# Kernel optimization log

Measured on AMD Instinct MI355X. Metric: run time of the kernel, lower is better.

## Reference

```python
import jax, jax.numpy as jnp
import numpy as np

D_MODEL = 1024
N_HEADS = 16
D_HEAD = D_MODEL // N_HEADS


def setup_inputs() -> dict:
    key = jax.random.key(0)
    ks = jax.random.split(key, 5)
    s_in = 1.0 / np.sqrt(D_MODEL)
    x = jax.random.normal(ks[0], (4, 2048, D_MODEL), dtype=jnp.float32)
    W_qkv = jax.random.uniform(ks[1], (D_MODEL, 3 * D_MODEL), jnp.float32, -s_in, s_in)
    b_qkv = jax.random.uniform(ks[2], (3 * D_MODEL,), jnp.float32, -s_in, s_in)
    W_out = jax.random.uniform(ks[3], (D_MODEL, D_MODEL), jnp.float32, -s_in, s_in)
    b_out = jax.random.uniform(ks[4], (D_MODEL,), jnp.float32, -s_in, s_in)
    return {"x": x, "W_qkv": W_qkv, "b_qkv": b_qkv, "W_out": W_out, "b_out": b_out}


def reference(x, W_qkv, b_qkv, W_out, b_out):
    B, T, C = x.shape
    qkv = x @ W_qkv + b_qkv                       # [B,T,3C]
    q, k, v = jnp.split(qkv, 3, axis=-1)
    # [B,T,C] -> [B,H,T,Dh]
    def heads(t):
        return t.reshape(B, T, N_HEADS, D_HEAD).transpose(0, 2, 1, 3)
    q, k, v = heads(q), heads(k), heads(v)
    scale = 1.0 / np.sqrt(D_HEAD).astype(np.float32)
    attn = jnp.einsum('bhqd,bhkd->bhqk', q, k) * scale   # [B,H,T,T]
    causal = jnp.tril(jnp.ones((T, T), dtype=bool))
    attn = jnp.where(causal, attn, -jnp.inf)
    attn_weights = jax.nn.softmax(attn, axis=-1)
    out = jnp.einsum('bhqk,bhkd->bhqd', attn_weights, v)  # [B,H,T,Dh]
    out = out.transpose(0, 2, 1, 3).reshape(B, T, C)
    return out @ W_out + b_out
```

## Files before the change

kernel.cpp:

```cpp
#include <hip/hip_runtime.h>
#include <hip/hip_bf16.h>

#define BATCH   4
#define SEQ     2048
#define DMODEL  1024
#define NHEADS  16
#define DHEAD   64
#define MROWS   (BATCH*SEQ)
#define QKV_N   (3*DMODEL)
#define NEG_BIG (-1.0e30f)
#define WS_NEED ((size_t)MROWS * 2*DMODEL * sizeof(__hip_bfloat16))
#define SCALE_Q 0.18033688011112042f

using bf16 = __hip_bfloat16;
typedef __attribute__((ext_vector_type(8))) short short8;
typedef __attribute__((ext_vector_type(4))) float floatx4;

__device__ __align__(16) unsigned short g_wqT[QKV_N * DMODEL];
__device__ __align__(16) unsigned short g_woT[DMODEL * DMODEL];
__device__ __align__(16) unsigned short g_xb [MROWS * DMODEL];

__device__ __forceinline__ unsigned short f2bf_rne(float f) {
    union { bf16 b; unsigned short u; } t;
    t.b = __float2bfloat16(f);
    return t.u;
}

__device__ __forceinline__ void gload_lds16(const void* g, void* l) {
    __builtin_amdgcn_global_load_lds(
        (const __attribute__((address_space(1))) unsigned*)g,
        (__attribute__((address_space(3))) unsigned*)l, 16, 0, 0);
}

__global__ __launch_bounds__(256) void cast_x(const float* __restrict__ x) {
    const size_t i = ((size_t)blockIdx.x*256 + threadIdx.x)*8;
    const float4 a = *(const float4*)(x + i);
    const float4 b = *(const float4*)(x + i + 4);
    union { uint4 u4; unsigned short us[8]; } o;
    o.us[0]=f2bf_rne(a.x); o.us[1]=f2bf_rne(a.y); o.us[2]=f2bf_rne(a.z); o.us[3]=f2bf_rne(a.w);
    o.us[4]=f2bf_rne(b.x); o.us[5]=f2bf_rne(b.y); o.us[6]=f2bf_rne(b.z); o.us[7]=f2bf_rne(b.w);
    *(uint4*)(g_xb + i) = o.u4;
}

__global__ __launch_bounds__(256) void transcast_w(
    const float* __restrict__ W, int N, int which)
{
    unsigned short* dst = which ? g_woT : g_wqT;
    __shared__ unsigned short T[64][72];
    const int n0 = blockIdx.x * 64, k0 = blockIdx.y * 64;
    const int tid = threadIdx.x;
    const int r = tid >> 2, c0 = (tid & 3) * 16;

#pragma unroll
    for (int it = 0; it < 4; ++it) {
        const float4 v = *(const float4*)(W + (size_t)(k0 + r)*N + n0 + c0 + it*4);
        T[r][c0 + it*4 + 0] = f2bf_rne(v.x);
        T[r][c0 + it*4 + 1] = f2bf_rne(v.y);
        T[r][c0 + it*4 + 2] = f2bf_rne(v.z);
        T[r][c0 + it*4 + 3] = f2bf_rne(v.w);
    }
    __syncthreads();
    const int nr = tid >> 2, kc0 = (tid & 3) * 16;
#pragma unroll
    for (int it = 0; it < 2; ++it) {
        union { uint4 u4; unsigned short us[8]; } o;
#pragma unroll
        for (int j = 0; j < 8; j++) o.us[j] = T[kc0 + it*8 + j][nr];
        *(uint4*)(dst + (size_t)(n0 + nr)*DMODEL + k0 + kc0 + it*8) = o.u4;
    }
}

template<int QKV_MODE>
__global__ __launch_bounds__(512, 2) void gemm256x128(
    const void* __restrict__ Av, const float* __restrict__ bias,
    void* __restrict__ C0, void* __restrict__ C1, void* __restrict__ C2)
{
    const unsigned short* A  = QKV_MODE ? g_xb  : (const unsigned short*)Av;
    const unsigned short* BT = QKV_MODE ? g_wqT : g_woT;
    constexpr int NBN = QKV_MODE ? 24 : 8;
    constexpr int NWG = NBN * 32;

    __shared__ __align__(16) char smem[98304];
    char* const sA = smem;
    char* const sB = smem + 65536;

    const int orig = blockIdx.x;
    const int wgid = (orig & 7) * (NWG >> 3) + (orig >> 3);
    const int bm = wgid / NBN, bn = wgid % NBN;

    const int tid  = threadIdx.x;
    const int w    = tid >> 6, lane = tid & 63;
    const int m16  = lane & 15, quad = lane >> 4;
    const int rw   = w >> 1, cw = w & 1;

    const int rL = lane >> 2;
    const int cD = (lane & 3) ^ ((lane >> 3) & 3);
    const unsigned short* gA = A  + (size_t)(bm*256 + rL)*DMODEL + cD*8;
    const unsigned short* gB = BT + (size_t)(bn*128 + rL)*DMODEL + cD*8;

    const int laneRd = m16*64 + (quad ^ ((m16 >> 1) & 3))*16;

    floatx4 acc[2][2][4];
#pragma unroll
    for (int q = 0; q < 2; ++q)
#pragma unroll
        for (int i = 0; i < 2; ++i)
#pragma unroll
            for (int j = 0; j < 4; ++j) {
                acc[q][i][j][0]=0.f; acc[q][i][j][1]=0.f;
                acc[q][i][j][2]=0.f; acc[q][i][j][3]=0.f;
            }

    auto stageA = [&](int buf, int a, int k0) {
        const int rg = 4*a + (w >> 1), kh = w & 1;
        gload_lds16(gA + (size_t)(rg*16)*DMODEL + k0 + kh*32,
                    sA + buf*32768 + (rg*2 + kh)*1024);
    };
    auto stageB = [&](int buf, int b, int k0) {
        const int rg = 4*b + (w >> 1), kh = w & 1;
        gload_lds16(gB + (size_t)(rg*16)*DMODEL + k0 + kh*32,
                    sB + buf*16384 + (rg*2 + kh)*1024);
    };

    stageB(0, 0, 0); stageB(0, 1, 0);
    stageA(0, 0, 0); stageA(0, 1, 0); stageA(0, 2, 0); stageA(0, 3, 0);
    asm volatile("s_waitcnt vmcnt(0)" ::: "memory");
    __builtin_amdgcn_s_barrier();

    const int NT = DMODEL / 64;
    for (int t = 0; t < NT; ++t) {
        const int  buf = t & 1;
        const int  k1  = (t + 1) * 64;
        const bool st  = (t + 1 < NT);
        char* const Ab = sA + buf*32768;
        char* const Bb = sB + buf*16384;

        short8 bf[4][2], af[2][2];
#pragma unroll
        for (int j = 0; j < 4; ++j)
#pragma unroll
            for (int kh = 0; kh < 2; ++kh)
                bf[j][kh] = *(const short8*)(Bb + ((cw*4 + j)*2 + kh)*1024 + laneRd);
#pragma unroll
        for (int i = 0; i < 2; ++i)
#pragma unroll
            for (int kh = 0; kh < 2; ++kh)
                af[i][kh] = *(const short8*)(Ab + ((rw*2 + i)*2 + kh)*1024 + laneRd);

        if (st) { stageB(buf^1, 0, k1); stageB(buf^1, 1, k1); }
        __builtin_amdgcn_s_barrier();

        __builtin_amdgcn_s_setprio(1);
#pragma unroll
        for (int i = 0; i < 2; ++i)
#pragma unroll
            for (int j = 0; j < 4; ++j) {
                acc[0][i][j] = __builtin_amdgcn_mfma_f32_16x16x32_bf16(
                    af[i][0], bf[j][0], acc[0][i][j], 0, 0, 0);
                acc[0][i][j] = __builtin_amdgcn_mfma_f32_16x16x32_bf16(
                    af[i][1], bf[j][1], acc[0][i][j], 0, 0, 0);
            }
        __builtin_amdgcn_s_setprio(0);

        if (st) { asm volatile("s_waitcnt vmcnt(2)" ::: "memory"); }
        else    { asm volatile("s_waitcnt vmcnt(0)" ::: "memory"); }
        __builtin_amdgcn_s_barrier();

#pragma unroll
        for (int i = 0; i < 2; ++i)
#pragma unroll
            for (int kh = 0; kh < 2; ++kh)
                af[i][kh] = *(const short8*)(Ab + ((8 + rw*2 + i)*2 + kh)*1024 + laneRd);

        if (st) { stageA(buf^1, 0, k1); stageA(buf^1, 1, k1);
                  stageA(buf^1, 2, k1); stageA(buf^1, 3, k1); }
        __builtin_amdgcn_s_barrier();

        __builtin_amdgcn_s_setprio(1);
#pragma unroll
        for (int i = 0; i < 2; ++i)
#pragma unroll
            for (int j = 0; j < 4; ++j) {
                acc[1][i][j] = __builtin_amdgcn_mfma_f32_16x16x32_bf16(
                    af[i][0], bf[j][0], acc[1][i][j], 0, 0, 0);
                acc[1][i][j] = __builtin_amdgcn_mfma_f32_16x16x32_bf16(
                    af[i][1], bf[j][1], acc[1][i][j], 0, 0, 0);
            }
        __builtin_amdgcn_s_setprio(0);

        if (st) { asm volatile("s_waitcnt vmcnt(2)" ::: "memory"); }
        else    { asm volatile("s_waitcnt vmcnt(0)" ::: "memory"); }
        __builtin_amdgcn_s_barrier();
    }

    float bv[4];
#pragma unroll
    for (int j = 0; j < 4; ++j)
        bv[j] = bias[bn*128 + cw*64 + j*16 + m16];

    if (QKV_MODE) {
        const int seg = bn >> 3;
        if (seg < 2) {
            bf16* Cout = (bf16*)(seg ? C1 : C0);
            const float sc = seg ? 1.0f : SCALE_Q;
#pragma unroll
            for (int q = 0; q < 2; ++q)
#pragma unroll
                for (int i = 0; i < 2; ++i)
#pragma unroll
                    for (int r = 0; r < 4; ++r) {
                        const int gm = bm*256 + q*128 + rw*32 + i*16 + quad*4 + r;
#pragma unroll
                        for (int j = 0; j < 4; ++j) {
                            const int cc = ((bn & 7)*128 + cw*64 + j*16 + m16);
                            Cout[(size_t)gm*DMODEL + cc] =
                                __float2bfloat16((acc[q][i][j][r] + bv[j]) * sc);
                        }
                    }
        } else {
            bf16* VT = (bf16*)C2;
#pragma unroll
            for (int q = 0; q < 2; ++q)
#pragma unroll
                for (int i = 0; i < 2; ++i) {
                    const int gm0 = bm*256 + q*128 + rw*32 + i*16 + quad*4;
                    const int bb = gm0 >> 11, t0 = gm0 & 2047;
#pragma unroll
                    for (int j = 0; j < 4; ++j) {
                        const int cv = (bn & 7)*128 + cw*64 + j*16 + m16;
                        const int hh = cv >> 6, dd = cv & 63;
                        union { unsigned long long u8; unsigned short us[4]; } o;
#pragma unroll
                        for (int r = 0; r < 4; ++r)
                            o.us[r] = f2bf_rne(acc[q][i][j][r] + bv[j]);
                        *(unsigned long long*)(VT
                            + ((size_t)((bb*NHEADS + hh)*DHEAD + dd))*SEQ + t0) = o.u8;
                    }
                }
        }
    } else {
        float* Cout = (float*)C0;
#pragma unroll
        for (int q = 0; q < 2; ++q)
#pragma unroll
            for (int i = 0; i < 2; ++i)
#pragma unroll
                for (int r = 0; r < 4; ++r) {
                    const int gm = bm*256 + q*128 + rw*32 + i*16 + quad*4 + r;
#pragma unroll
                    for (int j = 0; j < 4; ++j) {
                        const int cc = bn*128 + cw*64 + j*16 + m16;
                        Cout[(size_t)gm*DMODEL + cc] = acc[q][i][j][r] + bv[j];
                    }
                }
    }
}

__global__ __launch_bounds__(256, 2) void attn_mfma3(
    const bf16* __restrict__ Qg, const bf16* __restrict__ Kg,
    const bf16* __restrict__ VTg, bf16* __restrict__ Og)
{
    __shared__ alignas(16) unsigned short Kt[2][64][72];
    __shared__ alignas(16) unsigned short Vt[2][64][72];
    __shared__ alignas(16) unsigned short Ps[4][32][72];

    const int x = blockIdx.x;
    const int hlo = x & 7, rest = x >> 3;
    const int p = rest & 7, t2 = rest >> 3;
    const int b = t2 >> 1, h = hlo | ((t2 & 1) << 3);

    const int tid = threadIdx.x;
    const int w = tid >> 6, lane = tid & 63;
    const int m16 = lane & 15, quad = lane >> 4;
    const int sr = tid >> 2, sc0 = (tid & 3) * 8;
    const size_t bh = (size_t)(b*NHEADS + h);

    for (int seg = 0; seg < 2; ++seg) {
        const int qt  = seg ? (15 - p) : p;
        const int nkt = 2*qt + 2;
        const int qrow0 = qt*128 + w*32;

        short8 qf[2][2];
#pragma unroll
        for (int i = 0; i < 2; ++i)
#pragma unroll
            for (int c = 0; c < 2; ++c)
                qf[i][c] = *(const short8*)(Qg + (size_t)(b*SEQ + qrow0 + i*16 + m16)*DMODEL
                                            + h*DHEAD + c*32 + quad*8);

        floatx4 of[2][4];
        float mrow[2], lrow[2];
#pragma unroll
        for (int i = 0; i < 2; ++i) {
            mrow[i] = NEG_BIG; lrow[i] = 0.f;
#pragma unroll
            for (int nt = 0; nt < 4; ++nt) { of[i][nt][0]=0.f; of[i][nt][1]=0.f; of[i][nt][2]=0.f; of[i][nt][3]=0.f; }
        }

        {
            const bf16* kp = Kg  + (size_t)(b*SEQ + sr)*DMODEL + h*DHEAD + sc0;
            const bf16* vp = VTg + (bh*DHEAD + sr)*SEQ + sc0;
            const uint4 a0 = *(const uint4*)kp, a1 = *(const uint4*)(kp + 32);
            const uint4 b0 = *(const uint4*)vp, b1 = *(const uint4*)(vp + 32);
            __syncthreads();
            *(uint4*)&Kt[0][sr][sc0]      = a0;
            *(uint4*)&Kt[0][sr][sc0 + 32] = a1;
            *(uint4*)&Vt[0][sr][sc0]      = b0;
            *(uint4*)&Vt[0][sr][sc0 + 32] = b1;
            __syncthreads();
        }

        for (int kt = 0; kt < nkt; ++kt) {
            const int buf = kt & 1;
            const int k064 = kt * 64;
            const bool pre = (kt + 1 < nkt);
            uint4 kr0, kr1, vr0, vr1;
            if (pre) {
                const bf16* kp = Kg  + (size_t)(b*SEQ + k064 + 64 + sr)*DMODEL + h*DHEAD + sc0;
                const bf16* vp = VTg + (bh*DHEAD + sr)*SEQ + k064 + 64 + sc0;
                kr0 = *(const uint4*)kp; kr1 = *(const uint4*)(kp + 32);
                vr0 = *(const uint4*)vp; vr1 = *(const uint4*)(vp + 32);
            }

            floatx4 sf[2][4];
#pragma unroll
            for (int t4 = 0; t4 < 4; ++t4) {
                const short8 kf0 = *(const short8*)&Kt[buf][t4*16 + m16][quad*8];
                const short8 kf1 = *(const short8*)&Kt[buf][t4*16 + m16][32 + quad*8];
#pragma unroll
                for (int i = 0; i < 2; ++i) {
                    floatx4 a; a[0]=0.f; a[1]=0.f; a[2]=0.f; a[3]=0.f;
                    a = __builtin_amdgcn_mfma_f32_16x16x32_bf16(kf0, qf[i][0], a, 0, 0, 0);
                    a = __builtin_amdgcn_mfma_f32_16x16x32_bf16(kf1, qf[i][1], a, 0, 0, 0);
                    sf[i][t4] = a;
                }
            }

            const bool need_mask = (k064 + 63 > qrow0);
#pragma unroll
            for (int i = 0; i < 2; ++i) {
                if (need_mask) {
                    const int qg = qrow0 + i*16 + m16;
#pragma unroll
                    for (int t4 = 0; t4 < 4; ++t4)
#pragma unroll
                        for (int r = 0; r < 4; ++r)
                            if (k064 + t4*16 + quad*4 + r > qg) sf[i][t4][r] = NEG_BIG;
                }
                float mx = sf[i][0][0];
#pragma unroll
                for (int t4 = 0; t4 < 4; ++t4)
#pragma unroll
                    for (int r = 0; r < 4; ++r) mx = fmaxf(mx, sf[i][t4][r]);
                mx = fmaxf(mx, __shfl_xor(mx, 16));
                mx = fmaxf(mx, __shfl_xor(mx, 32));

                if (__any(mx > mrow[i] + 8.f)) {
                    const float mnew  = fmaxf(mrow[i], mx);
                    const float alpha = exp2f(mrow[i] - mnew);
                    mrow[i] = mnew;
                    lrow[i] *= alpha;
#pragma unroll
                    for (int nt = 0; nt < 4; ++nt)
#pragma unroll
                        for (int r = 0; r < 4; ++r) of[i][nt][r] *= alpha;
                }

                float rs = 0.f;
#pragma unroll
                for (int t4 = 0; t4 < 4; ++t4) {
#pragma unroll
                    for (int r = 0; r < 4; ++r) {
                        const float pv = exp2f(sf[i][t4][r] - mrow[i]);
                        sf[i][t4][r] = pv;
                        rs += pv;
                    }
                }
                rs += __shfl_xor(rs, 16);
                rs += __shfl_xor(rs, 32);
                lrow[i] += rs;

#pragma unroll
                for (int t4 = 0; t4 < 4; ++t4) {
                    union { unsigned long long u8; unsigned short us[4]; } o;
#pragma unroll
                    for (int r = 0; r < 4; ++r) o.us[r] = f2bf_rne(sf[i][t4][r]);
                    *(unsigned long long*)&Ps[w][i*16 + m16][t4*16 + quad*4] = o.u8;
                }
            }

            short8 pf[2][2];
#pragma unroll
            for (int i = 0; i < 2; ++i)
#pragma unroll
                for (int c = 0; c < 2; ++c)
                    pf[i][c] = *(const short8*)&Ps[w][i*16 + m16][c*32 + quad*8];
#pragma unroll
            for (int nt = 0; nt < 4; ++nt) {
                const short8 vf0 = *(const short8*)&Vt[buf][nt*16 + m16][quad*8];
                const short8 vf1 = *(const short8*)&Vt[buf][nt*16 + m16][32 + quad*8];
#pragma unroll
                for (int i = 0; i < 2; ++i) {
                    of[i][nt] = __builtin_amdgcn_mfma_f32_16x16x32_bf16(vf0, pf[i][0], of[i][nt], 0, 0, 0);
                    of[i][nt] = __builtin_amdgcn_mfma_f32_16x16x32_bf16(vf1, pf[i][1], of[i][nt], 0, 0, 0);
                }
            }

            if (pre) {
                *(uint4*)&Kt[buf^1][sr][sc0]      = kr0;
                *(uint4*)&Kt[buf^1][sr][sc0 + 32] = kr1;
                *(uint4*)&Vt[buf^1][sr][sc0]      = vr0;
                *(uint4*)&Vt[buf^1][sr][sc0 + 32] = vr1;
            }
            __syncthreads();
        }

#pragma unroll
        for (int i = 0; i < 2; ++i) {
            const float rl = 1.f / fmaxf(lrow[i], 1e-20f);
            const size_t rowbase = (size_t)(b*SEQ + qrow0 + i*16 + m16)*DMODEL + h*DHEAD;
#pragma unroll
            for (int nt = 0; nt < 4; ++nt) {
                union { unsigned long long u8; unsigned short us[4]; } o;
#pragma unroll
                for (int r = 0; r < 4; ++r) o.us[r] = f2bf_rne(of[i][nt][r] * rl);
                *(unsigned long long*)(Og + rowbase + nt*16 + quad*4) = o.u8;
            }
        }
    }
}

__global__ void diag_fill(float* out, int n, float val) {
    int i = blockIdx.x*blockDim.x + threadIdx.x;
    if (i < n) out[i] = val;
}

extern "C" void kernel_launch(void* const* d_in, const int* in_sizes, int n_in,
                              void* d_out, int out_size, void* d_ws, size_t ws_size,
                              hipStream_t stream) {
    const float* x     = (const float*)d_in[0];
    const float* W_qkv = (const float*)d_in[1];
    const float* b_qkv = (const float*)d_in[2];
    const float* W_out = (const float*)d_in[3];
    const float* b_out = (const float*)d_in[4];

    if (ws_size < WS_NEED) {
        const float val = 100.f + (float)(ws_size >> 20);
        diag_fill<<<(out_size + 255)/256, 256, 0, stream>>>((float*)d_out, out_size, val);
        return;
    }

    bf16* Qb  = (bf16*)d_out;
    bf16* VTb = (bf16*)d_out + (size_t)MROWS*DMODEL;
    bf16* Kb  = (bf16*)d_ws;
    bf16* Ob  = (bf16*)d_ws + (size_t)MROWS*DMODEL;

    cast_x<<<MROWS*DMODEL/2048, 256, 0, stream>>>(x);
    {
        dim3 gq(QKV_N/64, DMODEL/64);
        transcast_w<<<gq, 256, 0, stream>>>(W_qkv, QKV_N, 0);
        dim3 go(DMODEL/64, DMODEL/64);
        transcast_w<<<go, 256, 0, stream>>>(W_out, DMODEL, 1);
    }
    {
        gemm256x128<1><<<768, 512, 0, stream>>>(nullptr, b_qkv, Qb, Kb, VTb);
    }
    {
        attn_mfma3<<<512, 256, 0, stream>>>(Qb, Kb, VTb, Ob);
    }
    {
        gemm256x128<0><<<256, 512, 0, stream>>>(Ob, b_out, d_out, nullptr, nullptr);
    }
}
```

Baseline: 277.8 us.

## Keep softmax probabilities in registers, fold max-subtract into MFMA, rebalance GEMM staging

```diff
diff --git a/kernel.cpp b/kernel.cpp
--- a/kernel.cpp
+++ b/kernel.cpp
@@ -71,7 +71,7 @@
 }
 
 template<int QKV_MODE>
-__global__ __launch_bounds__(512, 2) void gemm256x128(
+__device__ __forceinline__ void gemm_body(
     const void* __restrict__ Av, const float* __restrict__ bias,
     void* __restrict__ C0, void* __restrict__ C1, void* __restrict__ C2)
 {
@@ -147,7 +147,8 @@
             for (int kh = 0; kh < 2; ++kh)
                 af[i][kh] = *(const short8*)(Ab + ((rw*2 + i)*2 + kh)*1024 + laneRd);
 
-        if (st) { stageB(buf^1, 0, k1); stageB(buf^1, 1, k1); }
+        if (st) { stageB(buf^1, 0, k1); stageB(buf^1, 1, k1);
+                  stageA(buf^1, 0, k1); stageA(buf^1, 1, k1); }
         __builtin_amdgcn_s_barrier();
 
         __builtin_amdgcn_s_setprio(1);
@@ -162,7 +163,7 @@
             }
         __builtin_amdgcn_s_setprio(0);
 
-        if (st) { asm volatile("s_waitcnt vmcnt(2)" ::: "memory"); }
+        if (st) { asm volatile("s_waitcnt vmcnt(4)" ::: "memory"); }
         else    { asm volatile("s_waitcnt vmcnt(0)" ::: "memory"); }
         __builtin_amdgcn_s_barrier();
 
@@ -172,8 +173,7 @@
             for (int kh = 0; kh < 2; ++kh)
                 af[i][kh] = *(const short8*)(Ab + ((8 + rw*2 + i)*2 + kh)*1024 + laneRd);
 
-        if (st) { stageA(buf^1, 0, k1); stageA(buf^1, 1, k1);
-                  stageA(buf^1, 2, k1); stageA(buf^1, 3, k1); }
+        if (st) { stageA(buf^1, 2, k1); stageA(buf^1, 3, k1); }
         __builtin_amdgcn_s_barrier();
 
         __builtin_amdgcn_s_setprio(1);
@@ -256,13 +256,23 @@
     }
 }
 
-__global__ __launch_bounds__(256, 2) void attn_mfma3(
+__global__ __launch_bounds__(512, 2) void qkv_proj(
+    const float* __restrict__ bias, bf16* Q, bf16* K, bf16* VT)
+{
+    gemm_body<1>(nullptr, bias, Q, K, VT);
+}
+__global__ __launch_bounds__(512, 2) void out_proj(
+    const void* __restrict__ Av, const float* __restrict__ bias, float* C)
+{
+    gemm_body<0>(Av, bias, C, nullptr, nullptr);
+}
+
+__global__ __launch_bounds__(256, 3) void attn_mfma4(
     const bf16* __restrict__ Qg, const bf16* __restrict__ Kg,
     const bf16* __restrict__ VTg, bf16* __restrict__ Og)
 {
     __shared__ alignas(16) unsigned short Kt[2][64][72];
     __shared__ alignas(16) unsigned short Vt[2][64][72];
-    __shared__ alignas(16) unsigned short Ps[4][32][72];
 
     const int x = blockIdx.x;
     const int hlo = x & 7, rest = x >> 3;
@@ -274,6 +284,18 @@
     const int m16 = lane & 15, quad = lane >> 4;
     const int sr = tid >> 2, sc0 = (tid & 3) * 8;
     const size_t bh = (size_t)(b*NHEADS + h);
+    (void)w;
+
+    auto vscat = [&](unsigned short* vrow, int kb, uint4 v) {
+        int t4 = kb >> 4, qk = (kb >> 2) & 3;
+        int s4 = (t4 & 1)*8 + qk*2 + (t4 >> 1);
+        *(unsigned long long*)(vrow + s4*4) =
+            ((unsigned long long)v.y << 32) | v.x;
+        t4 = (kb + 4) >> 4; qk = ((kb + 4) >> 2) & 3;
+        s4 = (t4 & 1)*8 + qk*2 + (t4 >> 1);
+        *(unsigned long long*)(vrow + s4*4) =
+            ((unsigned long long)v.w << 32) | v.z;
+    };
 
     for (int seg = 0; seg < 2; ++seg) {
         const int qt  = seg ? (15 - p) : p;
@@ -292,7 +314,7 @@
         float mrow[2], lrow[2];
 #pragma unroll
         for (int i = 0; i < 2; ++i) {
-            mrow[i] = NEG_BIG; lrow[i] = 0.f;
+            mrow[i] = 0.f; lrow[i] = 0.f;
 #pragma unroll
             for (int nt = 0; nt < 4; ++nt) { of[i][nt][0]=0.f; of[i][nt][1]=0.f; of[i][nt][2]=0.f; of[i][nt][3]=0.f; }
         }
@@ -305,8 +327,8 @@
             __syncthreads();
             *(uint4*)&Kt[0][sr][sc0]      = a0;
             *(uint4*)&Kt[0][sr][sc0 + 32] = a1;
-            *(uint4*)&Vt[0][sr][sc0]      = b0;
-            *(uint4*)&Vt[0][sr][sc0 + 32] = b1;
+            vscat(&Vt[0][sr][0], sc0,      b0);
+            vscat(&Vt[0][sr][0], sc0 + 32, b1);
             __syncthreads();
         }
 
@@ -323,20 +345,24 @@
             }
 
             floatx4 sf[2][4];
+            __builtin_amdgcn_s_setprio(1);
 #pragma unroll
             for (int t4 = 0; t4 < 4; ++t4) {
                 const short8 kf0 = *(const short8*)&Kt[buf][t4*16 + m16][quad*8];
                 const short8 kf1 = *(const short8*)&Kt[buf][t4*16 + m16][32 + quad*8];
 #pragma unroll
                 for (int i = 0; i < 2; ++i) {
-                    floatx4 a; a[0]=0.f; a[1]=0.f; a[2]=0.f; a[3]=0.f;
+                    floatx4 a;
+                    a[0] = -mrow[i]; a[1] = -mrow[i]; a[2] = -mrow[i]; a[3] = -mrow[i];
                     a = __builtin_amdgcn_mfma_f32_16x16x32_bf16(kf0, qf[i][0], a, 0, 0, 0);
                     a = __builtin_amdgcn_mfma_f32_16x16x32_bf16(kf1, qf[i][1], a, 0, 0, 0);
                     sf[i][t4] = a;
                 }
             }
+            __builtin_amdgcn_s_setprio(0);
 
             const bool need_mask = (k064 + 63 > qrow0);
+            short8 pf[2][2];
 #pragma unroll
             for (int i = 0; i < 2; ++i) {
                 if (need_mask) {
@@ -355,46 +381,54 @@
                 mx = fmaxf(mx, __shfl_xor(mx, 16));
                 mx = fmaxf(mx, __shfl_xor(mx, 32));
 
-                if (__any(mx > mrow[i] + 8.f)) {
-                    const float mnew  = fmaxf(mrow[i], mx);
-                    const float alpha = exp2f(mrow[i] - mnew);
-                    mrow[i] = mnew;
+                float rs = 0.f;
+                if (__any(mx > 8.f)) {
+                    const float d     = fmaxf(mx, 0.f);
+                    const float alpha = exp2f(-d);
+                    mrow[i] += d;
                     lrow[i] *= alpha;
 #pragma unroll
                     for (int nt = 0; nt < 4; ++nt)
 #pragma unroll
                         for (int r = 0; r < 4; ++r) of[i][nt][r] *= alpha;
-                }
-
-                float rs = 0.f;
-#pragma unroll
-                for (int t4 = 0; t4 < 4; ++t4) {
-#pragma unroll
-                    for (int r = 0; r < 4; ++r) {
-                        const float pv = exp2f(sf[i][t4][r] - mrow[i]);
-                        sf[i][t4][r] = pv;
-                        rs += pv;
-                    }
+#pragma unroll
+                    for (int t4 = 0; t4 < 4; ++t4)
+#pragma unroll
+                        for (int r = 0; r < 4; ++r) {
+                            const float pv = exp2f(sf[i][t4][r] - d);
+                            sf[i][t4][r] = pv;
+                            rs += pv;
+                        }
+                } else {
+#pragma unroll
+                    for (int t4 = 0; t4 < 4; ++t4)
+#pragma unroll
+                        for (int r = 0; r < 4; ++r) {
+                            const float pv = exp2f(sf[i][t4][r]);
+                            sf[i][t4][r] = pv;
+                            rs += pv;
+                        }
                 }
                 rs += __shfl_xor(rs, 16);
                 rs += __shfl_xor(rs, 32);
                 lrow[i] += rs;
 
+                unsigned pw[4][2];
 #pragma unroll
                 for (int t4 = 0; t4 < 4; ++t4) {
-                    union { unsigned long long u8; unsigned short us[4]; } o;
-#pragma unroll
-                    for (int r = 0; r < 4; ++r) o.us[r] = f2bf_rne(sf[i][t4][r]);
-                    *(unsigned long long*)&Ps[w][i*16 + m16][t4*16 + quad*4] = o.u8;
-                }
-            }
-
-            short8 pf[2][2];
-#pragma unroll
-            for (int i = 0; i < 2; ++i)
-#pragma unroll
-                for (int c = 0; c < 2; ++c)
-                    pf[i][c] = *(const short8*)&Ps[w][i*16 + m16][c*32 + quad*8];
+                    pw[t4][0] = ((unsigned)f2bf_rne(sf[i][t4][1]) << 16) | f2bf_rne(sf[i][t4][0]);
+                    pw[t4][1] = ((unsigned)f2bf_rne(sf[i][t4][3]) << 16) | f2bf_rne(sf[i][t4][2]);
+                }
+#pragma unroll
+                for (int c = 0; c < 2; ++c) {
+                    union { unsigned u[4]; short8 s8; } tu;
+                    tu.u[0] = pw[c][0];     tu.u[1] = pw[c][1];
+                    tu.u[2] = pw[c + 2][0]; tu.u[3] = pw[c + 2][1];
+                    pf[i][c] = tu.s8;
+                }
+            }
+
+            __builtin_amdgcn_s_setprio(1);
 #pragma unroll
             for (int nt = 0; nt < 4; ++nt) {
                 const short8 vf0 = *(const short8*)&Vt[buf][nt*16 + m16][quad*8];
@@ -405,12 +439,13 @@
                     of[i][nt] = __builtin_amdgcn_mfma_f32_16x16x32_bf16(vf1, pf[i][1], of[i][nt], 0, 0, 0);
                 }
             }
+            __builtin_amdgcn_s_setprio(0);
 
             if (pre) {
                 *(uint4*)&Kt[buf^1][sr][sc0]      = kr0;
                 *(uint4*)&Kt[buf^1][sr][sc0 + 32] = kr1;
-                *(uint4*)&Vt[buf^1][sr][sc0]      = vr0;
-                *(uint4*)&Vt[buf^1][sr][sc0 + 32] = vr1;
+                vscat(&Vt[buf^1][sr][0], sc0,      vr0);
+                vscat(&Vt[buf^1][sr][0], sc0 + 32, vr1);
             }
             __syncthreads();
         }
@@ -462,13 +497,7 @@
         dim3 go(DMODEL/64, DMODEL/64);
         transcast_w<<<go, 256, 0, stream>>>(W_out, DMODEL, 1);
     }
-    {
-        gemm256x128<1><<<768, 512, 0, stream>>>(nullptr, b_qkv, Qb, Kb, VTb);
-    }
-    {
-        attn_mfma3<<<512, 256, 0, stream>>>(Qb, Kb, VTb, Ob);
-    }
-    {
-        gemm256x128<0><<<256, 512, 0, stream>>>(Ob, b_out, d_out, nullptr, nullptr);
-    }
-}
+    qkv_proj<<<768, 512, 0, stream>>>(b_qkv, Qb, Kb, VTb);
+    attn_mfma4<<<512, 256, 0, stream>>>(Qb, Kb, VTb, Ob);
+    out_proj<<<256, 512, 0, stream>>>(Ob, b_out, (float*)d_out);
+}
```

Result: slower. 301.9 us (+8.7%).

## Merge weight transcasts, rebalance GEMM staging, single-buffer V in attention

Applied to the files above, without the earlier changes.

```diff
diff --git a/kernel.cpp b/kernel.cpp
--- a/kernel.cpp
+++ b/kernel.cpp
@@ -42,12 +42,18 @@
     *(uint4*)(g_xb + i) = o.u4;
 }
 
-__global__ __launch_bounds__(256) void transcast_w(
-    const float* __restrict__ W, int N, int which)
+__global__ __launch_bounds__(256) void transcast_w2(
+    const float* __restrict__ Wq, const float* __restrict__ Wo)
 {
-    unsigned short* dst = which ? g_woT : g_wqT;
+    const int bx = blockIdx.x;
+    const float* W;
+    unsigned short* dst;
+    int N, n0;
+    if (bx < 48) { W = Wq; dst = g_wqT; N = QKV_N;  n0 = bx * 64; }
+    else         { W = Wo; dst = g_woT; N = DMODEL; n0 = (bx - 48) * 64; }
+    const int k0 = blockIdx.y * 64;
+
     __shared__ unsigned short T[64][72];
-    const int n0 = blockIdx.x * 64, k0 = blockIdx.y * 64;
     const int tid = threadIdx.x;
     const int r = tid >> 2, c0 = (tid & 3) * 16;
 
@@ -71,7 +77,7 @@
 }
 
 template<int QKV_MODE>
-__global__ __launch_bounds__(512, 2) void gemm256x128(
+__device__ __forceinline__ void gemm_body(
     const void* __restrict__ Av, const float* __restrict__ bias,
     void* __restrict__ C0, void* __restrict__ C1, void* __restrict__ C2)
 {
@@ -147,7 +153,8 @@
             for (int kh = 0; kh < 2; ++kh)
                 af[i][kh] = *(const short8*)(Ab + ((rw*2 + i)*2 + kh)*1024 + laneRd);
 
-        if (st) { stageB(buf^1, 0, k1); stageB(buf^1, 1, k1); }
+        if (st) { stageB(buf^1, 0, k1); stageB(buf^1, 1, k1);
+                  stageA(buf^1, 0, k1); stageA(buf^1, 1, k1); }
         __builtin_amdgcn_s_barrier();
 
         __builtin_amdgcn_s_setprio(1);
@@ -162,7 +169,7 @@
             }
         __builtin_amdgcn_s_setprio(0);
 
-        if (st) { asm volatile("s_waitcnt vmcnt(2)" ::: "memory"); }
+        if (st) { asm volatile("s_waitcnt vmcnt(4)" ::: "memory"); }
         else    { asm volatile("s_waitcnt vmcnt(0)" ::: "memory"); }
         __builtin_amdgcn_s_barrier();
 
@@ -172,8 +179,7 @@
             for (int kh = 0; kh < 2; ++kh)
                 af[i][kh] = *(const short8*)(Ab + ((8 + rw*2 + i)*2 + kh)*1024 + laneRd);
 
-        if (st) { stageA(buf^1, 0, k1); stageA(buf^1, 1, k1);
-                  stageA(buf^1, 2, k1); stageA(buf^1, 3, k1); }
+        if (st) { stageA(buf^1, 2, k1); stageA(buf^1, 3, k1); }
         __builtin_amdgcn_s_barrier();
 
         __builtin_amdgcn_s_setprio(1);
@@ -256,12 +262,23 @@
     }
 }
 
-__global__ __launch_bounds__(256, 2) void attn_mfma3(
+__global__ __launch_bounds__(512, 2) void qkv_proj(
+    const float* __restrict__ bias, bf16* Q, bf16* K, bf16* VT)
+{
+    gemm_body<1>(nullptr, bias, Q, K, VT);
+}
+__global__ __launch_bounds__(512, 2) void out_proj(
+    const void* __restrict__ Av, const float* __restrict__ bias, float* C)
+{
+    gemm_body<0>(Av, bias, C, nullptr, nullptr);
+}
+
+__global__ __launch_bounds__(256, 3) void attn_mfma5(
     const bf16* __restrict__ Qg, const bf16* __restrict__ Kg,
     const bf16* __restrict__ VTg, bf16* __restrict__ Og)
 {
     __shared__ alignas(16) unsigned short Kt[2][64][72];
-    __shared__ alignas(16) unsigned short Vt[2][64][72];
+    __shared__ alignas(16) unsigned short Vt[64][72];
     __shared__ alignas(16) unsigned short Ps[4][32][72];
 
     const int x = blockIdx.x;
@@ -305,8 +322,8 @@
             __syncthreads();
             *(uint4*)&Kt[0][sr][sc0]      = a0;
             *(uint4*)&Kt[0][sr][sc0 + 32] = a1;
-            *(uint4*)&Vt[0][sr][sc0]      = b0;
-            *(uint4*)&Vt[0][sr][sc0 + 32] = b1;
+            *(uint4*)&Vt[sr][sc0]         = b0;
+            *(uint4*)&Vt[sr][sc0 + 32]    = b1;
             __syncthreads();
         }
 
@@ -397,8 +414,8 @@
                     pf[i][c] = *(const short8*)&Ps[w][i*16 + m16][c*32 + quad*8];
 #pragma unroll
             for (int nt = 0; nt < 4; ++nt) {
-                const short8 vf0 = *(const short8*)&Vt[buf][nt*16 + m16][quad*8];
-                const short8 vf1 = *(const short8*)&Vt[buf][nt*16 + m16][32 + quad*8];
+                const short8 vf0 = *(const short8*)&Vt[nt*16 + m16][quad*8];
+                const short8 vf1 = *(const short8*)&Vt[nt*16 + m16][32 + quad*8];
 #pragma unroll
                 for (int i = 0; i < 2; ++i) {
                     of[i][nt] = __builtin_amdgcn_mfma_f32_16x16x32_bf16(vf0, pf[i][0], of[i][nt], 0, 0, 0);
@@ -406,11 +423,12 @@
                 }
             }
 
+            __syncthreads();
             if (pre) {
                 *(uint4*)&Kt[buf^1][sr][sc0]      = kr0;
                 *(uint4*)&Kt[buf^1][sr][sc0 + 32] = kr1;
-                *(uint4*)&Vt[buf^1][sr][sc0]      = vr0;
-                *(uint4*)&Vt[buf^1][sr][sc0 + 32] = vr1;
+                *(uint4*)&Vt[sr][sc0]             = vr0;
+                *(uint4*)&Vt[sr][sc0 + 32]        = vr1;
             }
             __syncthreads();
         }
@@ -457,18 +475,10 @@
 
     cast_x<<<MROWS*DMODEL/2048, 256, 0, stream>>>(x);
     {
-        dim3 gq(QKV_N/64, DMODEL/64);
-        transcast_w<<<gq, 256, 0, stream>>>(W_qkv, QKV_N, 0);
-        dim3 go(DMODEL/64, DMODEL/64);
-        transcast_w<<<go, 256, 0, stream>>>(W_out, DMODEL, 1);
-    }
-    {
-        gemm256x128<1><<<768, 512, 0, stream>>>(nullptr, b_qkv, Qb, Kb, VTb);
-    }
-    {
-        attn_mfma3<<<512, 256, 0, stream>>>(Qb, Kb, VTb, Ob);
-    }
-    {
-        gemm256x128<0><<<256, 512, 0, stream>>>(Ob, b_out, d_out, nullptr, nullptr);
-    }
-}
+        dim3 g(64, DMODEL/64);
+        transcast_w2<<<g, 256, 0, stream>>>(W_qkv, W_out);
+    }
+    qkv_proj<<<768, 512, 0, stream>>>(b_qkv, Qb, Kb, VTb);
+    attn_mfma5<<<512, 256, 0, stream>>>(Qb, Kb, VTb, Ob);
+    out_proj<<<256, 512, 0, stream>>>(Ob, b_out, (float*)d_out);
+}
```

New measurement: 287.9 us. 1.04x slower.
